# Performance work log

Hardware: AMD Instinct MI355X
Metric: run time of the kernel (lower is better)

## Reference

```python
import jax, jax.numpy as jnp
import numpy as np

DIM = 1024
DIM_HEAD = 128
HEADS = 8
DIM_INNER = DIM_HEAD * HEADS


def setup_inputs() -> dict:
    key = jax.random.key(0)
    k_x, k_qkv, k_out = jax.random.split(key, 3)
    x = jax.random.normal(k_x, (2, 2048, DIM), dtype=jnp.float32)
    gamma = jnp.ones((DIM,), dtype=jnp.float32)
    # nn.Linear weights stored as [out, in]; init ~ U(-1/sqrt(in), 1/sqrt(in))
    w_qkv = jax.random.uniform(k_qkv, (DIM_INNER * 3, DIM), dtype=jnp.float32,
                               minval=-1.0, maxval=1.0) / np.sqrt(DIM)
    w_out = jax.random.uniform(k_out, (DIM, DIM_INNER), dtype=jnp.float32,
                               minval=-1.0, maxval=1.0) / np.sqrt(DIM_INNER)
    return {"x": x, "gamma": gamma, "w_qkv": w_qkv, "w_out": w_out}


def reference(x, gamma, w_qkv, w_out):
    scale_norm = DIM ** 0.5
    scale_attn = DIM_HEAD ** -0.5
    # RMSNorm as written: F.normalize (L2) * sqrt(dim) * gamma
    l2 = jnp.sqrt(jnp.sum(x * x, axis=-1, keepdims=True))
    xn = x / jnp.maximum(l2, 1e-12) * scale_norm * gamma
    # QKV projection: [b, n, 3*h*d]
    qkv = jnp.einsum('bnc,fc->bnf', xn, w_qkv)
    b, n, _ = qkv.shape
    qkv = qkv.reshape(b, n, 3, HEADS, DIM_HEAD)
    q, k, v = (qkv[:, :, 0], qkv[:, :, 1], qkv[:, :, 2])  # [b, n, h, d]
    q = q * scale_attn
    sim = jnp.einsum('bihd,bjhd->bhij', q, k)
    causal_mask = jnp.triu(jnp.ones((n, n), dtype=bool), k=1)
    neg = -jnp.finfo(sim.dtype).max
    sim = jnp.where(causal_mask, neg, sim)
    attn = jax.nn.softmax(sim, axis=-1)
    out = jnp.einsum('bhij,bjhd->bihd', attn, v)
    out = out.reshape(b, n, DIM_INNER)  # merge heads: b n (h d)
    return jnp.einsum('bnf,cf->bnc', out, w_out)
```

## Files before the change

### kernel.cpp

```cpp
#include <hip/hip_runtime.h>

#define SEQ 2048
#define NTOK 4096
#define DIM 1024
#define FQKV 3072
#define SC_Q (0.08838834764831843f * 1.4426950408889634f)
#define SC_NORM 32.0f

typedef short short8 __attribute__((ext_vector_type(8)));
typedef float f32x4 __attribute__((ext_vector_type(4)));
typedef unsigned short u16x4 __attribute__((ext_vector_type(4)));

__device__ __forceinline__ unsigned short f2bf(float f) {
    unsigned int u = __float_as_uint(f);
    u += 0x7fffu + ((u >> 16) & 1u);
    return (unsigned short)(u >> 16);
}
__device__ __forceinline__ float bf2f(unsigned short b) {
    return __uint_as_float(((unsigned int)b) << 16);
}
__device__ __forceinline__ void gl_lds16(const void* g, void* l) {
    __builtin_amdgcn_global_load_lds((const __attribute__((address_space(1))) void*)g,
                                     (__attribute__((address_space(3))) void*)l, 16, 0, 0);
}

__global__ __launch_bounds__(256) void prep(const float* __restrict__ x,
                                            const float* __restrict__ gamma,
                                            unsigned short* __restrict__ xn,
                                            const float* __restrict__ wq,
                                            unsigned short* __restrict__ wqb,
                                            const float* __restrict__ wo,
                                            unsigned short* __restrict__ wob) {
    if (blockIdx.x < 4096) {
        int token = blockIdx.x;
        float4 v = ((const float4*)(x + (size_t)token * DIM))[threadIdx.x];
        float ss = v.x * v.x + v.y * v.y + v.z * v.z + v.w * v.w;
#pragma unroll
        for (int off = 32; off > 0; off >>= 1) ss += __shfl_down(ss, off);
        __shared__ float wsum[4];
        if ((threadIdx.x & 63) == 0) wsum[threadIdx.x >> 6] = ss;
        __syncthreads();
        float tot = wsum[0] + wsum[1] + wsum[2] + wsum[3];
        float sc = SC_NORM / fmaxf(sqrtf(tot), 1e-12f);
        float4 g = ((const float4*)gamma)[threadIdx.x];
        u16x4 o;
        o.x = f2bf(v.x * sc * g.x);
        o.y = f2bf(v.y * sc * g.y);
        o.z = f2bf(v.z * sc * g.z);
        o.w = f2bf(v.w * sc * g.w);
        ((u16x4*)(xn + (size_t)token * DIM))[threadIdx.x] = o;
    } else {
        int i = (blockIdx.x - 4096) * 256 + threadIdx.x;
        const float* w; unsigned short* o; int idx;
        if (i < 786432) { w = wq; o = wqb; idx = i; }
        else            { w = wo; o = wob; idx = i - 786432; }
        float4 v = ((const float4*)w)[idx];
        u16x4 r;
        r.x = f2bf(v.x); r.y = f2bf(v.y); r.z = f2bf(v.z); r.w = f2bf(v.w);
        ((u16x4*)o)[idx] = r;
    }
}

template<int C_MODE, int TM>
__global__ __launch_bounds__(256) void gemm_bf16(const unsigned short* __restrict__ A,
                                                 const unsigned short* __restrict__ B,
                                                 void* __restrict__ Cv,
                                                 int M, int N, int K) {
    constexpr int MF = TM / 32;
    __shared__ unsigned short As[TM * 64];
    __shared__ unsigned short Bs[128 * 64];

    int lin = blockIdx.y * gridDim.x + blockIdx.x;
    int nwg = gridDim.x * gridDim.y;
    int w = (lin & 7) * (nwg >> 3) + (lin >> 3);
    int bx = w % gridDim.x, by = w / gridDim.x;

    const int bn = bx * 128, bm = by * TM;
    const int tid = threadIdx.x, lane = tid & 63, wv = tid >> 6;
    const int wr = wv >> 1, wc = wv & 1;
    const int l15 = lane & 15, g = lane >> 4;

    f32x4 acc[MF][4] = {};

    auto stage = [&](int k0) {
#pragma unroll
        for (int ia = 0; ia < TM / 32; ++ia) {
            int ci = ia * 256 + wv * 64 + lane;
            int row = ci >> 3, cc = ci & 7;
            int co = (cc ^ (row & 7)) << 3;
            gl_lds16(A + (size_t)(bm + row) * K + k0 + co, &As[(ia * 256 + wv * 64) * 8]);
        }
#pragma unroll
        for (int ib = 0; ib < 4; ++ib) {
            int ci = ib * 256 + wv * 64 + lane;
            int row = ci >> 3, cc = ci & 7;
            int co = (cc ^ (row & 7)) << 3;
            gl_lds16(B + (size_t)(bn + row) * K + k0 + co, &Bs[(ib * 256 + wv * 64) * 8]);
        }
    };

    stage(0);
    asm volatile("s_waitcnt vmcnt(0)\ns_barrier" ::: "memory");

    for (int k0 = 0; k0 < K; k0 += 64) {
        short8 af[2][MF], bf[2][4];
#pragma unroll
        for (int ks = 0; ks < 2; ++ks) {
#pragma unroll
            for (int f = 0; f < MF; ++f) {
                int ra = wr * (TM / 2) + f * 16 + l15;
                af[ks][f] = *(const short8*)&As[ra * 64 + (((ks * 4 + g) ^ (ra & 7)) << 3)];
            }
#pragma unroll
            for (int f = 0; f < 4; ++f) {
                int rb = wc * 64 + f * 16 + l15;
                bf[ks][f] = *(const short8*)&Bs[rb * 64 + (((ks * 4 + g) ^ (rb & 7)) << 3)];
            }
        }
        asm volatile("s_waitcnt lgkmcnt(0)\ns_barrier" ::: "memory");
        if (k0 + 64 < K) stage(k0 + 64);
#pragma unroll
        for (int ks = 0; ks < 2; ++ks)
#pragma unroll
            for (int i = 0; i < MF; ++i)
#pragma unroll
                for (int j = 0; j < 4; ++j)
                    acc[i][j] = __builtin_amdgcn_mfma_f32_16x16x32_bf16(af[ks][i], bf[ks][j], acc[i][j], 0, 0, 0);
        asm volatile("s_waitcnt vmcnt(0)\ns_barrier" ::: "memory");
    }

    if (C_MODE == 0) {
        float* C = (float*)Cv;
#pragma unroll
        for (int i = 0; i < MF; ++i)
#pragma unroll
            for (int j = 0; j < 4; ++j)
#pragma unroll
                for (int v = 0; v < 4; ++v) {
                    int row = bm + wr * (TM / 2) + i * 16 + g * 4 + v;
                    int col = bn + wc * 64 + j * 16 + l15;
                    C[(size_t)row * N + col] = acc[i][j][v];
                }
    } else {
        unsigned short* C = (unsigned short*)Cv;
        float s = (bn < 1024) ? SC_Q : 1.0f;
#pragma unroll
        for (int i = 0; i < MF; ++i)
#pragma unroll
            for (int j = 0; j < 4; ++j)
#pragma unroll
                for (int v = 0; v < 4; ++v) {
                    int row = bm + wr * (TM / 2) + i * 16 + g * 4 + v;
                    int col = bn + wc * 64 + j * 16 + l15;
                    C[(size_t)row * N + col] = f2bf(acc[i][j][v] * s);
                }
    }
}

__global__ __launch_bounds__(256) void transpose_v(const unsigned short* __restrict__ qkv,
                                                   unsigned short* __restrict__ vt) {
    __shared__ unsigned short T[64][72];
    const int t0 = blockIdx.x * 64, d0 = blockIdx.y * 64, bh = blockIdx.z;
    const int b = bh >> 3, h = bh & 7;
    const int tid = threadIdx.x;
#pragma unroll
    for (int p = 0; p < 2; ++p) {
        int r = p * 32 + (tid >> 3), c = tid & 7;
        *(short8*)&T[r][c * 8] =
            *(const short8*)(qkv + (size_t)(b * SEQ + t0 + r) * FQKV + 2048 + h * 128 + d0 + c * 8);
    }
    __syncthreads();
#pragma unroll
    for (int p = 0; p < 2; ++p) {
        int d = p * 32 + (tid >> 3), c = tid & 7;
        short8 v;
#pragma unroll
        for (int j = 0; j < 8; ++j) v[j] = (short)T[c * 8 + j][d];
        *(short8*)(vt + (size_t)(bh * 128 + d0 + d) * SEQ + t0 + c * 8) = v;
    }
}

__global__ __launch_bounds__(256) void attn_mfma(const unsigned short* __restrict__ qkv,
                                                 const unsigned short* __restrict__ vt,
                                                 unsigned short* __restrict__ ao,
                                                 unsigned short* __restrict__ po,
                                                 float* __restrict__ pml) {
    __shared__ unsigned short Ks[64 * 128];
    __shared__ unsigned short Vs[128 * 64];
    __shared__ unsigned short Ps[4][16 * 64];
    const int h = blockIdx.y, b = blockIdx.z;
    const int x = blockIdx.x;
    int qblk, s, nsp;
    if (x < 30)      { qblk = 27 - x / 3;               s = x % 3;  nsp = 3; }
    else if (x < 46) { int i = x - 30; qblk = 31 - (i >> 2); s = i & 3; nsp = 4; }
    else if (x < 64) { int i = x - 46; qblk = 17 - (i >> 1); s = i & 1; nsp = 2; }
    else             { qblk = 72 - x;                   s = 0;      nsp = 1; }
    const int T = qblk + 1;
    const int jb0 = (s * T) / nsp, jb1 = ((s + 1) * T) / nsp;
    const int split = (nsp > 1);
    const int slot = ((b * 8 + h) << 6) + x;

    const int tid = threadIdx.x, lane = tid & 63, wv = tid >> 6;
    const int l15 = lane & 15, g = lane >> 4;
    const int q0 = qblk * 64;
    const int qrow = q0 + wv * 16 + l15;

    auto stageK = [&](int jb) {
#pragma unroll
        for (int inst = 0; inst < 4; ++inst) {
            int ci = inst * 256 + wv * 64 + lane;
            int rowk = ci >> 4, ck = ci & 15;
            gl_lds16(qkv + (size_t)(b * SEQ + jb * 64 + rowk) * FQKV + 1024 + h * 128
                         + ((ck ^ (rowk & 7)) << 3),
                     &Ks[(inst * 256 + wv * 64) * 8]);
        }
    };
    auto stageV = [&](int jb) {
#pragma unroll
        for (int inst = 0; inst < 4; ++inst) {
            int ci = inst * 256 + wv * 64 + lane;
            int rowv = ci >> 3, cv = ci & 7;
            gl_lds16(vt + (size_t)((b * 8 + h) * 128 + rowv) * SEQ + jb * 64
                        + ((cv ^ (rowv & 7)) << 3),
                     &Vs[(inst * 256 + wv * 64) * 8]);
        }
    };

    short8 qf[4];
    {
        const unsigned short* qb = qkv + (size_t)(b * SEQ + qrow) * FQKV + h * 128;
#pragma unroll
        for (int ks = 0; ks < 4; ++ks) qf[ks] = *(const short8*)(qb + ks * 32 + g * 8);
    }

    float m_r = -1e30f, l_r = 0.f;
    f32x4 o[8] = {};

    stageK(jb0);
    __syncthreads();

    for (int jb = jb0; jb < jb1; ++jb) {
        stageV(jb);

        f32x4 sv[4] = {};
        __builtin_amdgcn_s_setprio(1);
#pragma unroll
        for (int ks = 0; ks < 4; ++ks) {
#pragma unroll
            for (int fi = 0; fi < 4; ++fi) {
                int rk = fi * 16 + l15;
                short8 kf = *(const short8*)&Ks[rk * 128 + (((ks * 4 + g) ^ (rk & 7)) << 3)];
                sv[fi] = __builtin_amdgcn_mfma_f32_16x16x32_bf16(kf, qf[ks], sv[fi], 0, 0, 0);
            }
        }
        __builtin_amdgcn_s_setprio(0);

        if (jb == qblk) {
#pragma unroll
            for (int fi = 0; fi < 4; ++fi)
#pragma unroll
                for (int v = 0; v < 4; ++v) {
                    int kv = q0 + fi * 16 + g * 4 + v;
                    if (kv > qrow) sv[fi][v] = -1e30f;
                }
        }

        float mx = -1e30f;
#pragma unroll
        for (int fi = 0; fi < 4; ++fi)
            mx = fmaxf(mx, fmaxf(fmaxf(sv[fi][0], sv[fi][1]), fmaxf(sv[fi][2], sv[fi][3])));
        mx = fmaxf(mx, __shfl_xor(mx, 16));
        mx = fmaxf(mx, __shfl_xor(mx, 32));
        if (__any(mx - m_r > 16.0f)) {
            float Mn = fmaxf(m_r, mx);
            float alpha = exp2f(m_r - Mn);
            l_r *= alpha;
            float av[4];
#pragma unroll
            for (int v = 0; v < 4; ++v) av[v] = __shfl(alpha, g * 4 + v);
#pragma unroll
            for (int fn = 0; fn < 8; ++fn) {
                o[fn][0] *= av[0]; o[fn][1] *= av[1]; o[fn][2] *= av[2]; o[fn][3] *= av[3];
            }
            m_r = Mn;
        }

        float ps = 0.f;
#pragma unroll
        for (int fi = 0; fi < 4; ++fi) {
#pragma unroll
            for (int p2 = 0; p2 < 2; ++p2) {
                float e0 = exp2f(sv[fi][2 * p2] - m_r);
                float e1 = exp2f(sv[fi][2 * p2 + 1] - m_r);
                ps += e0 + e1;
                unsigned short b0 = f2bf(e0), b1 = f2bf(e1);
                int kv = fi * 16 + g * 4 + 2 * p2;
                int addr = l15 * 64 + (((kv >> 3) ^ (l15 & 7)) << 3) + (kv & 7);
                *(unsigned int*)&Ps[wv][addr] = (unsigned int)b0 | ((unsigned int)b1 << 16);
            }
        }
        ps += __shfl_xor(ps, 16);
        ps += __shfl_xor(ps, 32);
        l_r += ps;

        __syncthreads();
        if (jb + 1 < jb1) stageK(jb + 1);

        __builtin_amdgcn_s_setprio(1);
#pragma unroll
        for (int ks = 0; ks < 2; ++ks) {
            short8 pa = *(const short8*)&Ps[wv][l15 * 64 + (((ks * 4 + g) ^ (l15 & 7)) << 3)];
#pragma unroll
            for (int fn = 0; fn < 8; ++fn) {
                int rv = fn * 16 + l15;
                short8 vf = *(const short8*)&Vs[rv * 64 + (((ks * 4 + g) ^ (rv & 7)) << 3)];
                o[fn] = __builtin_amdgcn_mfma_f32_16x16x32_bf16(pa, vf, o[fn], 0, 0, 0);
            }
        }
        __builtin_amdgcn_s_setprio(0);

        __syncthreads();
    }

    if (split) {
        unsigned short* od = po + (size_t)slot * 8192;
#pragma unroll
        for (int fn = 0; fn < 8; ++fn)
#pragma unroll
            for (int v = 0; v < 4; ++v)
                od[(wv * 16 + g * 4 + v) * 128 + fn * 16 + l15] = f2bf(o[fn][v]);
        if (g == 0) {
            pml[(size_t)slot * 128 + wv * 16 + l15] = m_r;
            pml[(size_t)slot * 128 + 64 + wv * 16 + l15] = l_r;
        }
    } else {
        float lv[4];
#pragma unroll
        for (int v = 0; v < 4; ++v) lv[v] = 1.0f / __shfl(l_r, g * 4 + v);
#pragma unroll
        for (int fn = 0; fn < 8; ++fn)
#pragma unroll
            for (int v = 0; v < 4; ++v) {
                int row = b * SEQ + q0 + wv * 16 + g * 4 + v;
                ao[(size_t)row * DIM + h * 128 + fn * 16 + l15] = f2bf(o[fn][v] * lv[v]);
            }
    }
}

__global__ __launch_bounds__(256) void attn_combine(const unsigned short* __restrict__ po,
                                                    const float* __restrict__ pml,
                                                    unsigned short* __restrict__ ao) {
    const int qblk = 9 + blockIdx.x, h = blockIdx.y, b = blockIdx.z;
    int base, n;
    if (qblk >= 28)      { base = 30 + (31 - qblk) * 4; n = 4; }
    else if (qblk >= 18) { base = (27 - qblk) * 3;      n = 3; }
    else                 { base = 46 + (17 - qblk) * 2; n = 2; }
    const int slot0 = ((b * 8 + h) << 6) + base;
    const int row = threadIdx.x >> 2, dp = threadIdx.x & 3;

    float M = -1e30f;
#pragma unroll
    for (int s2 = 0; s2 < 4; ++s2)
        if (s2 < n) M = fmaxf(M, pml[(size_t)(slot0 + s2) * 128 + row]);
    float denom = 0.f;
#pragma unroll
    for (int s2 = 0; s2 < 4; ++s2)
        if (s2 < n) denom += exp2f(pml[(size_t)(slot0 + s2) * 128 + row] - M)
                             * pml[(size_t)(slot0 + s2) * 128 + 64 + row];
    float inv = 1.0f / denom;

    float acc[32] = {};
#pragma unroll
    for (int s2 = 0; s2 < 4; ++s2)
        if (s2 < n) {
            float wgt = exp2f(pml[(size_t)(slot0 + s2) * 128 + row] - M) * inv;
            const unsigned short* ob = po + (size_t)(slot0 + s2) * 8192 + row * 128 + dp * 32;
#pragma unroll
            for (int j = 0; j < 4; ++j) {
                short8 pv = *(const short8*)(ob + j * 8);
#pragma unroll
                for (int e = 0; e < 8; ++e)
                    acc[j * 8 + e] += wgt * bf2f((unsigned short)pv[e]);
            }
        }

    unsigned short* dst = ao + ((size_t)(b * SEQ + qblk * 64 + row)) * DIM + h * 128 + dp * 32;
#pragma unroll
    for (int j = 0; j < 4; ++j) {
        short8 r;
#pragma unroll
        for (int e = 0; e < 8; ++e) r[e] = (short)f2bf(acc[j * 8 + e]);
        *(short8*)(dst + j * 8) = r;
    }
}

extern "C" void kernel_launch(void* const* d_in, const int* in_sizes, int n_in,
                              void* d_out, int out_size, void* d_ws, size_t ws_size,
                              hipStream_t stream) {
    const float* x     = (const float*)d_in[0];
    const float* gamma = (const float*)d_in[1];
    const float* w_qkv = (const float*)d_in[2];
    const float* w_out = (const float*)d_in[3];

    char* ws = (char*)d_ws;
    unsigned short* qkvb = (unsigned short*)ws;
    unsigned short* vtb  = (unsigned short*)(ws + 25165824);
    unsigned short* xnb  = (unsigned short*)(ws + 33554432);
    unsigned short* wqb  = (unsigned short*)(ws + 41943040);
    unsigned short* wob  = (unsigned short*)(ws + 48234496);
    unsigned short* aob  = (unsigned short*)(ws + 50331648);
    float*          pml  = (float*)(ws + 41943040);
    unsigned short* po   = (unsigned short*)d_out;

    prep<<<8192, 256, 0, stream>>>(x, gamma, xnb, w_qkv, wqb, w_out, wob);
    gemm_bf16<1, 128><<<dim3(24, 32), 256, 0, stream>>>(xnb, wqb, qkvb, NTOK, FQKV, DIM);
    transpose_v<<<dim3(32, 2, 16), 256, 0, stream>>>(qkvb, vtb);
    attn_mfma<<<dim3(73, 8, 2), 256, 0, stream>>>(qkvb, vtb, aob, po, pml);
    attn_combine<<<dim3(23, 8, 2), 256, 0, stream>>>(po, pml, aob);
    gemm_bf16<0, 64><<<dim3(8, 64), 256, 0, stream>>>(aob, wob, (float*)d_out, NTOK, DIM, DIM);
}
```

Measured before the change: 118.2 us.

## Process 128 query rows per attention block to reuse staged K/V tiles

Each attention workgroup now handles two 64-row query subtiles (128 rows) instead of one, so each K and V tile staged in LDS feeds twice as many MFMAs. The split-K schedule and the combine kernel are remapped to 128-row super-blocks, with 36 blocks per head instead of 73. This halves K/V global-to-LDS traffic per query row. In exchange it doubles accumulator registers, which may lower occupancy, and yields fewer, coarser blocks, which may hurt load balance. It also does some extra causal masking work on the diagonal tiles.

```diff
diff --git a/kernel.cpp b/kernel.cpp
--- a/kernel.cpp
+++ b/kernel.cpp
@@ -187,23 +187,21 @@
                                                  float* __restrict__ pml) {
     __shared__ unsigned short Ks[64 * 128];
     __shared__ unsigned short Vs[128 * 64];
-    __shared__ unsigned short Ps[4][16 * 64];
+    __shared__ unsigned short Ps[4][2][16 * 64];
     const int h = blockIdx.y, b = blockIdx.z;
     const int x = blockIdx.x;
-    int qblk, s, nsp;
-    if (x < 30)      { qblk = 27 - x / 3;               s = x % 3;  nsp = 3; }
-    else if (x < 46) { int i = x - 30; qblk = 31 - (i >> 2); s = i & 3; nsp = 4; }
-    else if (x < 64) { int i = x - 46; qblk = 17 - (i >> 1); s = i & 1; nsp = 2; }
-    else             { qblk = 72 - x;                   s = 0;      nsp = 1; }
-    const int T = qblk + 1;
+    int qsb, s, nsp;
+    if (x < 24)      { qsb = 15 - x / 3;               s = x % 3;  nsp = 3; }
+    else if (x < 32) { int i = x - 24; qsb = 7 - (i >> 1); s = i & 1; nsp = 2; }
+    else             { qsb = 35 - x;                   s = 0;      nsp = 1; }
+    const int T = 2 * qsb + 2;
     const int jb0 = (s * T) / nsp, jb1 = ((s + 1) * T) / nsp;
     const int split = (nsp > 1);
-    const int slot = ((b * 8 + h) << 6) + x;
+    const int slot = ((b * 8 + h) << 5) + x;
 
     const int tid = threadIdx.x, lane = tid & 63, wv = tid >> 6;
     const int l15 = lane & 15, g = lane >> 4;
-    const int q0 = qblk * 64;
-    const int qrow = q0 + wv * 16 + l15;
+    const int q0 = qsb * 128;
 
     auto stageK = [&](int jb) {
 #pragma unroll
@@ -226,15 +224,16 @@
         }
     };
 
-    short8 qf[4];
-    {
-        const unsigned short* qb = qkv + (size_t)(b * SEQ + qrow) * FQKV + h * 128;
-#pragma unroll
-        for (int ks = 0; ks < 4; ++ks) qf[ks] = *(const short8*)(qb + ks * 32 + g * 8);
-    }
-
-    float m_r = -1e30f, l_r = 0.f;
-    f32x4 o[8] = {};
+    short8 qf[2][4];
+#pragma unroll
+    for (int e = 0; e < 2; ++e) {
+        const unsigned short* qb = qkv + (size_t)(b * SEQ + q0 + wv * 16 + e * 64 + l15) * FQKV + h * 128;
+#pragma unroll
+        for (int ks = 0; ks < 4; ++ks) qf[e][ks] = *(const short8*)(qb + ks * 32 + g * 8);
+    }
+
+    float m_r[2] = {-1e30f, -1e30f}, l_r[2] = {0.f, 0.f};
+    f32x4 o[2][8] = {};
 
     stageK(jb0);
     __syncthreads();
@@ -242,7 +241,7 @@
     for (int jb = jb0; jb < jb1; ++jb) {
         stageV(jb);
 
-        f32x4 sv[4] = {};
+        f32x4 sv[2][4] = {};
         __builtin_amdgcn_s_setprio(1);
 #pragma unroll
         for (int ks = 0; ks < 4; ++ks) {
@@ -250,58 +249,66 @@
             for (int fi = 0; fi < 4; ++fi) {
                 int rk = fi * 16 + l15;
                 short8 kf = *(const short8*)&Ks[rk * 128 + (((ks * 4 + g) ^ (rk & 7)) << 3)];
-                sv[fi] = __builtin_amdgcn_mfma_f32_16x16x32_bf16(kf, qf[ks], sv[fi], 0, 0, 0);
+                sv[0][fi] = __builtin_amdgcn_mfma_f32_16x16x32_bf16(kf, qf[0][ks], sv[0][fi], 0, 0, 0);
+                sv[1][fi] = __builtin_amdgcn_mfma_f32_16x16x32_bf16(kf, qf[1][ks], sv[1][fi], 0, 0, 0);
             }
         }
         __builtin_amdgcn_s_setprio(0);
 
-        if (jb == qblk) {
+        if (jb >= 2 * qsb) {
+#pragma unroll
+            for (int e = 0; e < 2; ++e) {
+                int qrow = q0 + wv * 16 + e * 64 + l15;
+#pragma unroll
+                for (int fi = 0; fi < 4; ++fi)
+#pragma unroll
+                    for (int v = 0; v < 4; ++v) {
+                        int kv = jb * 64 + fi * 16 + g * 4 + v;
+                        if (kv > qrow) sv[e][fi][v] = -1e30f;
+                    }
+            }
+        }
+
+#pragma unroll
+        for (int e = 0; e < 2; ++e) {
+            float mx = -1e30f;
 #pragma unroll
             for (int fi = 0; fi < 4; ++fi)
-#pragma unroll
-                for (int v = 0; v < 4; ++v) {
-                    int kv = q0 + fi * 16 + g * 4 + v;
-                    if (kv > qrow) sv[fi][v] = -1e30f;
+                mx = fmaxf(mx, fmaxf(fmaxf(sv[e][fi][0], sv[e][fi][1]), fmaxf(sv[e][fi][2], sv[e][fi][3])));
+            mx = fmaxf(mx, __shfl_xor(mx, 16));
+            mx = fmaxf(mx, __shfl_xor(mx, 32));
+            if (__any(mx - m_r[e] > 16.0f)) {
+                float Mn = fmaxf(m_r[e], mx);
+                float alpha = exp2f(m_r[e] - Mn);
+                l_r[e] *= alpha;
+                float av[4];
+#pragma unroll
+                for (int v = 0; v < 4; ++v) av[v] = __shfl(alpha, g * 4 + v);
+#pragma unroll
+                for (int fn = 0; fn < 8; ++fn) {
+                    o[e][fn][0] *= av[0]; o[e][fn][1] *= av[1];
+                    o[e][fn][2] *= av[2]; o[e][fn][3] *= av[3];
                 }
-        }
-
-        float mx = -1e30f;
-#pragma unroll
-        for (int fi = 0; fi < 4; ++fi)
-            mx = fmaxf(mx, fmaxf(fmaxf(sv[fi][0], sv[fi][1]), fmaxf(sv[fi][2], sv[fi][3])));
-        mx = fmaxf(mx, __shfl_xor(mx, 16));
-        mx = fmaxf(mx, __shfl_xor(mx, 32));
-        if (__any(mx - m_r > 16.0f)) {
-            float Mn = fmaxf(m_r, mx);
-            float alpha = exp2f(m_r - Mn);
-            l_r *= alpha;
-            float av[4];
-#pragma unroll
-            for (int v = 0; v < 4; ++v) av[v] = __shfl(alpha, g * 4 + v);
-#pragma unroll
-            for (int fn = 0; fn < 8; ++fn) {
-                o[fn][0] *= av[0]; o[fn][1] *= av[1]; o[fn][2] *= av[2]; o[fn][3] *= av[3];
-            }
-            m_r = Mn;
-        }
-
-        float ps = 0.f;
-#pragma unroll
-        for (int fi = 0; fi < 4; ++fi) {
-#pragma unroll
-            for (int p2 = 0; p2 < 2; ++p2) {
-                float e0 = exp2f(sv[fi][2 * p2] - m_r);
-                float e1 = exp2f(sv[fi][2 * p2 + 1] - m_r);
-                ps += e0 + e1;
-                unsigned short b0 = f2bf(e0), b1 = f2bf(e1);
-                int kv = fi * 16 + g * 4 + 2 * p2;
-                int addr = l15 * 64 + (((kv >> 3) ^ (l15 & 7)) << 3) + (kv & 7);
-                *(unsigned int*)&Ps[wv][addr] = (unsigned int)b0 | ((unsigned int)b1 << 16);
-            }
-        }
-        ps += __shfl_xor(ps, 16);
-        ps += __shfl_xor(ps, 32);
-        l_r += ps;
+                m_r[e] = Mn;
+            }
+            float ps = 0.f;
+#pragma unroll
+            for (int fi = 0; fi < 4; ++fi) {
+#pragma unroll
+                for (int p2 = 0; p2 < 2; ++p2) {
+                    float e0 = exp2f(sv[e][fi][2 * p2] - m_r[e]);
+                    float e1 = exp2f(sv[e][fi][2 * p2 + 1] - m_r[e]);
+                    ps += e0 + e1;
+                    unsigned short b0 = f2bf(e0), b1 = f2bf(e1);
+                    int kv = fi * 16 + g * 4 + 2 * p2;
+                    int addr = l15 * 64 + (((kv >> 3) ^ (l15 & 7)) << 3) + (kv & 7);
+                    *(unsigned int*)&Ps[wv][e][addr] = (unsigned int)b0 | ((unsigned int)b1 << 16);
+                }
+            }
+            ps += __shfl_xor(ps, 16);
+            ps += __shfl_xor(ps, 32);
+            l_r[e] += ps;
+        }
 
         __syncthreads();
         if (jb + 1 < jb1) stageK(jb + 1);
@@ -309,12 +316,14 @@
         __builtin_amdgcn_s_setprio(1);
 #pragma unroll
         for (int ks = 0; ks < 2; ++ks) {
-            short8 pa = *(const short8*)&Ps[wv][l15 * 64 + (((ks * 4 + g) ^ (l15 & 7)) << 3)];
+            short8 pa0 = *(const short8*)&Ps[wv][0][l15 * 64 + (((ks * 4 + g) ^ (l15 & 7)) << 3)];
+            short8 pa1 = *(const short8*)&Ps[wv][1][l15 * 64 + (((ks * 4 + g) ^ (l15 & 7)) << 3)];
 #pragma unroll
             for (int fn = 0; fn < 8; ++fn) {
                 int rv = fn * 16 + l15;
                 short8 vf = *(const short8*)&Vs[rv * 64 + (((ks * 4 + g) ^ (rv & 7)) << 3)];
-                o[fn] = __builtin_amdgcn_mfma_f32_16x16x32_bf16(pa, vf, o[fn], 0, 0, 0);
+                o[0][fn] = __builtin_amdgcn_mfma_f32_16x16x32_bf16(pa0, vf, o[0][fn], 0, 0, 0);
+                o[1][fn] = __builtin_amdgcn_mfma_f32_16x16x32_bf16(pa1, vf, o[1][fn], 0, 0, 0);
             }
         }
         __builtin_amdgcn_s_setprio(0);
@@ -323,60 +332,67 @@
     }
 
     if (split) {
-        unsigned short* od = po + (size_t)slot * 8192;
-#pragma unroll
-        for (int fn = 0; fn < 8; ++fn)
-#pragma unroll
-            for (int v = 0; v < 4; ++v)
-                od[(wv * 16 + g * 4 + v) * 128 + fn * 16 + l15] = f2bf(o[fn][v]);
+        unsigned short* od = po + (size_t)slot * 16384;
+#pragma unroll
+        for (int e = 0; e < 2; ++e)
+#pragma unroll
+            for (int fn = 0; fn < 8; ++fn)
+#pragma unroll
+                for (int v = 0; v < 4; ++v)
+                    od[(wv * 16 + e * 64 + g * 4 + v) * 128 + fn * 16 + l15] = f2bf(o[e][fn][v]);
         if (g == 0) {
-            pml[(size_t)slot * 128 + wv * 16 + l15] = m_r;
-            pml[(size_t)slot * 128 + 64 + wv * 16 + l15] = l_r;
+#pragma unroll
+            for (int e = 0; e < 2; ++e) {
+                pml[(size_t)slot * 256 + wv * 16 + e * 64 + l15] = m_r[e];
+                pml[(size_t)slot * 256 + 128 + wv * 16 + e * 64 + l15] = l_r[e];
+            }
         }
     } else {
-        float lv[4];
-#pragma unroll
-        for (int v = 0; v < 4; ++v) lv[v] = 1.0f / __shfl(l_r, g * 4 + v);
-#pragma unroll
-        for (int fn = 0; fn < 8; ++fn)
-#pragma unroll
-            for (int v = 0; v < 4; ++v) {
-                int row = b * SEQ + q0 + wv * 16 + g * 4 + v;
-                ao[(size_t)row * DIM + h * 128 + fn * 16 + l15] = f2bf(o[fn][v] * lv[v]);
-            }
+#pragma unroll
+        for (int e = 0; e < 2; ++e) {
+            float lv[4];
+#pragma unroll
+            for (int v = 0; v < 4; ++v) lv[v] = 1.0f / __shfl(l_r[e], g * 4 + v);
+#pragma unroll
+            for (int fn = 0; fn < 8; ++fn)
+#pragma unroll
+                for (int v = 0; v < 4; ++v) {
+                    int row = b * SEQ + q0 + wv * 16 + e * 64 + g * 4 + v;
+                    ao[(size_t)row * DIM + h * 128 + fn * 16 + l15] = f2bf(o[e][fn][v] * lv[v]);
+                }
+        }
     }
 }
 
 __global__ __launch_bounds__(256) void attn_combine(const unsigned short* __restrict__ po,
                                                     const float* __restrict__ pml,
                                                     unsigned short* __restrict__ ao) {
-    const int qblk = 9 + blockIdx.x, h = blockIdx.y, b = blockIdx.z;
+    const int qsb = 4 + blockIdx.x, h = blockIdx.y, b = blockIdx.z;
     int base, n;
-    if (qblk >= 28)      { base = 30 + (31 - qblk) * 4; n = 4; }
-    else if (qblk >= 18) { base = (27 - qblk) * 3;      n = 3; }
-    else                 { base = 46 + (17 - qblk) * 2; n = 2; }
-    const int slot0 = ((b * 8 + h) << 6) + base;
-    const int row = threadIdx.x >> 2, dp = threadIdx.x & 3;
+    if (qsb >= 8) { base = (15 - qsb) * 3;      n = 3; }
+    else          { base = 24 + (7 - qsb) * 2;  n = 2; }
+    const int slot0 = ((b * 8 + h) << 5) + base;
+    const int row = threadIdx.x >> 1, d0 = (threadIdx.x & 1) * 64;
 
     float M = -1e30f;
 #pragma unroll
-    for (int s2 = 0; s2 < 4; ++s2)
-        if (s2 < n) M = fmaxf(M, pml[(size_t)(slot0 + s2) * 128 + row]);
+    for (int s2 = 0; s2 < 3; ++s2)
+        if (s2 < n) M = fmaxf(M, pml[(size_t)(slot0 + s2) * 256 + row]);
     float denom = 0.f;
 #pragma unroll
-    for (int s2 = 0; s2 < 4; ++s2)
-        if (s2 < n) denom += exp2f(pml[(size_t)(slot0 + s2) * 128 + row] - M)
-                             * pml[(size_t)(slot0 + s2) * 128 + 64 + row];
+    for (int s2 = 0; s2 < 3; ++s2)
+        if (s2 < n) denom += exp2f(pml[(size_t)(slot0 + s2) * 256 + row] - M)
+                             * pml[(size_t)(slot0 + s2) * 256 + 128 + row];
     float inv = 1.0f / denom;
 
-    float acc[32] = {};
-#pragma unroll
-    for (int s2 = 0; s2 < 4; ++s2)
+    float acc[64] = {};
+#pragma unroll
+    for (int s2 = 0; s2 < 3; ++s2)
         if (s2 < n) {
-            float wgt = exp2f(pml[(size_t)(slot0 + s2) * 128 + row] - M) * inv;
-            const unsigned short* ob = po + (size_t)(slot0 + s2) * 8192 + row * 128 + dp * 32;
-#pragma unroll
-            for (int j = 0; j < 4; ++j) {
+            float wgt = exp2f(pml[(size_t)(slot0 + s2) * 256 + row] - M) * inv;
+            const unsigned short* ob = po + (size_t)(slot0 + s2) * 16384 + row * 128 + d0;
+#pragma unroll
+            for (int j = 0; j < 8; ++j) {
                 short8 pv = *(const short8*)(ob + j * 8);
 #pragma unroll
                 for (int e = 0; e < 8; ++e)
@@ -384,9 +400,9 @@
             }
         }
 
-    unsigned short* dst = ao + ((size_t)(b * SEQ + qblk * 64 + row)) * DIM + h * 128 + dp * 32;
-#pragma unroll
-    for (int j = 0; j < 4; ++j) {
+    unsigned short* dst = ao + ((size_t)(b * SEQ + qsb * 128 + row)) * DIM + h * 128 + d0;
+#pragma unroll
+    for (int j = 0; j < 8; ++j) {
         short8 r;
 #pragma unroll
         for (int e = 0; e < 8; ++e) r[e] = (short)f2bf(acc[j * 8 + e]);
@@ -415,7 +431,7 @@
     prep<<<8192, 256, 0, stream>>>(x, gamma, xnb, w_qkv, wqb, w_out, wob);
     gemm_bf16<1, 128><<<dim3(24, 32), 256, 0, stream>>>(xnb, wqb, qkvb, NTOK, FQKV, DIM);
     transpose_v<<<dim3(32, 2, 16), 256, 0, stream>>>(qkvb, vtb);
-    attn_mfma<<<dim3(73, 8, 2), 256, 0, stream>>>(qkvb, vtb, aob, po, pml);
-    attn_combine<<<dim3(23, 8, 2), 256, 0, stream>>>(po, pml, aob);
+    attn_mfma<<<dim3(36, 8, 2), 256, 0, stream>>>(qkvb, vtb, aob, po, pml);
+    attn_combine<<<dim3(12, 8, 2), 256, 0, stream>>>(po, pml, aob);
     gemm_bf16<0, 64><<<dim3(8, 64), 256, 0, stream>>>(aob, wob, (float*)d_out, NTOK, DIM, DIM);
 }
```

Result: slower. 144.4 us (+22.2%).

## Switch attention to 32x32x16 MFMA with two waves per block

Applied to the files above, without the earlier changes.

The attention kernel moves from 16x16x32 to 32x32x16 bf16 MFMA tiles, using 2 waves of 32 query rows each instead of 4 waves of 16. This reduces per-wave LDS traffic for K/V fragments and removes the cross-lane shuffles for max, sum and alpha, since each lane now owns one query row. It also packs P with v_cvt_pk_bf16_f32 and stores outputs as packed pairs. The cost is fewer threads per block staging K/V tiles, more accumulator registers per lane, and a different XOR-swizzled P layout in LDS.

```diff
diff --git a/kernel.cpp b/kernel.cpp
--- a/kernel.cpp
+++ b/kernel.cpp
@@ -9,6 +9,7 @@
 
 typedef short short8 __attribute__((ext_vector_type(8)));
 typedef float f32x4 __attribute__((ext_vector_type(4)));
+typedef float f32x16 __attribute__((ext_vector_type(16)));
 typedef unsigned short u16x4 __attribute__((ext_vector_type(4)));
 
 __device__ __forceinline__ unsigned short f2bf(float f) {
@@ -180,14 +181,14 @@
     }
 }
 
-__global__ __launch_bounds__(256) void attn_mfma(const unsigned short* __restrict__ qkv,
+__global__ __launch_bounds__(128) void attn_mfma(const unsigned short* __restrict__ qkv,
                                                  const unsigned short* __restrict__ vt,
                                                  unsigned short* __restrict__ ao,
                                                  unsigned short* __restrict__ po,
                                                  float* __restrict__ pml) {
     __shared__ unsigned short Ks[64 * 128];
     __shared__ unsigned short Vs[128 * 64];
-    __shared__ unsigned short Ps[4][16 * 64];
+    __shared__ unsigned int Ps[2][32 * 32];
     const int h = blockIdx.y, b = blockIdx.z;
     const int x = blockIdx.x;
     int qblk, s, nsp;
@@ -201,40 +202,40 @@
     const int slot = ((b * 8 + h) << 6) + x;
 
     const int tid = threadIdx.x, lane = tid & 63, wv = tid >> 6;
-    const int l15 = lane & 15, g = lane >> 4;
+    const int q = lane & 31, hi = lane >> 5;
     const int q0 = qblk * 64;
-    const int qrow = q0 + wv * 16 + l15;
+    const int qrow = q0 + wv * 32 + q;
 
     auto stageK = [&](int jb) {
 #pragma unroll
-        for (int inst = 0; inst < 4; ++inst) {
-            int ci = inst * 256 + wv * 64 + lane;
+        for (int inst = 0; inst < 8; ++inst) {
+            int ci = inst * 128 + tid;
             int rowk = ci >> 4, ck = ci & 15;
             gl_lds16(qkv + (size_t)(b * SEQ + jb * 64 + rowk) * FQKV + 1024 + h * 128
                          + ((ck ^ (rowk & 7)) << 3),
-                     &Ks[(inst * 256 + wv * 64) * 8]);
+                     &Ks[ci * 8]);
         }
     };
     auto stageV = [&](int jb) {
 #pragma unroll
-        for (int inst = 0; inst < 4; ++inst) {
-            int ci = inst * 256 + wv * 64 + lane;
+        for (int inst = 0; inst < 8; ++inst) {
+            int ci = inst * 128 + tid;
             int rowv = ci >> 3, cv = ci & 7;
             gl_lds16(vt + (size_t)((b * 8 + h) * 128 + rowv) * SEQ + jb * 64
                         + ((cv ^ (rowv & 7)) << 3),
-                     &Vs[(inst * 256 + wv * 64) * 8]);
+                     &Vs[ci * 8]);
         }
     };
 
-    short8 qf[4];
+    short8 qf[8];
     {
         const unsigned short* qb = qkv + (size_t)(b * SEQ + qrow) * FQKV + h * 128;
 #pragma unroll
-        for (int ks = 0; ks < 4; ++ks) qf[ks] = *(const short8*)(qb + ks * 32 + g * 8);
+        for (int ks = 0; ks < 8; ++ks) qf[ks] = *(const short8*)(qb + ks * 16 + hi * 8);
     }
 
     float m_r = -1e30f, l_r = 0.f;
-    f32x4 o[8] = {};
+    f32x16 o[4] = {};
 
     stageK(jb0);
     __syncthreads();
@@ -242,64 +243,60 @@
     for (int jb = jb0; jb < jb1; ++jb) {
         stageV(jb);
 
-        f32x4 sv[4] = {};
+        f32x16 sv[2] = {};
         __builtin_amdgcn_s_setprio(1);
 #pragma unroll
-        for (int ks = 0; ks < 4; ++ks) {
-#pragma unroll
-            for (int fi = 0; fi < 4; ++fi) {
-                int rk = fi * 16 + l15;
-                short8 kf = *(const short8*)&Ks[rk * 128 + (((ks * 4 + g) ^ (rk & 7)) << 3)];
-                sv[fi] = __builtin_amdgcn_mfma_f32_16x16x32_bf16(kf, qf[ks], sv[fi], 0, 0, 0);
+        for (int ks = 0; ks < 8; ++ks) {
+#pragma unroll
+            for (int fi = 0; fi < 2; ++fi) {
+                int rk = fi * 32 + q;
+                short8 kf = *(const short8*)&Ks[rk * 128 + (((ks * 2 + hi) ^ (rk & 7)) << 3)];
+                sv[fi] = __builtin_amdgcn_mfma_f32_32x32x16_bf16(kf, qf[ks], sv[fi], 0, 0, 0);
             }
         }
         __builtin_amdgcn_s_setprio(0);
 
         if (jb == qblk) {
 #pragma unroll
-            for (int fi = 0; fi < 4; ++fi)
-#pragma unroll
-                for (int v = 0; v < 4; ++v) {
-                    int kv = q0 + fi * 16 + g * 4 + v;
-                    if (kv > qrow) sv[fi][v] = -1e30f;
+            for (int fi = 0; fi < 2; ++fi)
+#pragma unroll
+                for (int r = 0; r < 16; ++r) {
+                    int kv = jb * 64 + fi * 32 + (r & 3) + 8 * (r >> 2) + 4 * hi;
+                    if (kv > qrow) sv[fi][r] = -1e30f;
                 }
         }
 
         float mx = -1e30f;
 #pragma unroll
-        for (int fi = 0; fi < 4; ++fi)
-            mx = fmaxf(mx, fmaxf(fmaxf(sv[fi][0], sv[fi][1]), fmaxf(sv[fi][2], sv[fi][3])));
-        mx = fmaxf(mx, __shfl_xor(mx, 16));
+        for (int fi = 0; fi < 2; ++fi)
+#pragma unroll
+            for (int r = 0; r < 16; ++r) mx = fmaxf(mx, sv[fi][r]);
         mx = fmaxf(mx, __shfl_xor(mx, 32));
         if (__any(mx - m_r > 16.0f)) {
             float Mn = fmaxf(m_r, mx);
             float alpha = exp2f(m_r - Mn);
             l_r *= alpha;
-            float av[4];
-#pragma unroll
-            for (int v = 0; v < 4; ++v) av[v] = __shfl(alpha, g * 4 + v);
-#pragma unroll
-            for (int fn = 0; fn < 8; ++fn) {
-                o[fn][0] *= av[0]; o[fn][1] *= av[1]; o[fn][2] *= av[2]; o[fn][3] *= av[3];
-            }
+#pragma unroll
+            for (int fd = 0; fd < 4; ++fd)
+#pragma unroll
+                for (int r = 0; r < 16; ++r) o[fd][r] *= alpha;
             m_r = Mn;
         }
 
         float ps = 0.f;
 #pragma unroll
-        for (int fi = 0; fi < 4; ++fi) {
-#pragma unroll
-            for (int p2 = 0; p2 < 2; ++p2) {
-                float e0 = exp2f(sv[fi][2 * p2] - m_r);
-                float e1 = exp2f(sv[fi][2 * p2 + 1] - m_r);
+        for (int fi = 0; fi < 2; ++fi) {
+#pragma unroll
+            for (int rp = 0; rp < 8; ++rp) {
+                float e0 = exp2f(sv[fi][2 * rp] - m_r);
+                float e1 = exp2f(sv[fi][2 * rp + 1] - m_r);
                 ps += e0 + e1;
-                unsigned short b0 = f2bf(e0), b1 = f2bf(e1);
-                int kv = fi * 16 + g * 4 + 2 * p2;
-                int addr = l15 * 64 + (((kv >> 3) ^ (l15 & 7)) << 3) + (kv & 7);
-                *(unsigned int*)&Ps[wv][addr] = (unsigned int)b0 | ((unsigned int)b1 << 16);
-            }
-        }
-        ps += __shfl_xor(ps, 16);
+                unsigned int pk;
+                asm("v_cvt_pk_bf16_f32 %0, %1, %2" : "=v"(pk) : "v"(e0), "v"(e1));
+                int kvp = (rp & 1) + ((rp >> 1) << 2) + 2 * hi + fi * 16;
+                Ps[wv][q * 32 + (kvp ^ ((q & 7) << 2))] = pk;
+            }
+        }
         ps += __shfl_xor(ps, 32);
         l_r += ps;
 
@@ -308,13 +305,14 @@
 
         __builtin_amdgcn_s_setprio(1);
 #pragma unroll
-        for (int ks = 0; ks < 2; ++ks) {
-            short8 pa = *(const short8*)&Ps[wv][l15 * 64 + (((ks * 4 + g) ^ (l15 & 7)) << 3)];
-#pragma unroll
-            for (int fn = 0; fn < 8; ++fn) {
-                int rv = fn * 16 + l15;
-                short8 vf = *(const short8*)&Vs[rv * 64 + (((ks * 4 + g) ^ (rv & 7)) << 3)];
-                o[fn] = __builtin_amdgcn_mfma_f32_16x16x32_bf16(pa, vf, o[fn], 0, 0, 0);
+        for (int c = 0; c < 4; ++c) {
+            short8 pb = *(const short8*)((const unsigned short*)
+                            &Ps[wv][q * 32 + (((c * 8 + hi * 4)) ^ ((q & 7) << 2))]);
+#pragma unroll
+            for (int fd = 0; fd < 4; ++fd) {
+                int rv = fd * 32 + q;
+                short8 vf = *(const short8*)&Vs[rv * 64 + (((c * 2 + hi) ^ (rv & 7)) << 3)];
+                o[fd] = __builtin_amdgcn_mfma_f32_32x32x16_bf16(vf, pb, o[fd], 0, 0, 0);
             }
         }
         __builtin_amdgcn_s_setprio(0);
@@ -325,24 +323,31 @@
     if (split) {
         unsigned short* od = po + (size_t)slot * 8192;
 #pragma unroll
-        for (int fn = 0; fn < 8; ++fn)
-#pragma unroll
-            for (int v = 0; v < 4; ++v)
-                od[(wv * 16 + g * 4 + v) * 128 + fn * 16 + l15] = f2bf(o[fn][v]);
-        if (g == 0) {
-            pml[(size_t)slot * 128 + wv * 16 + l15] = m_r;
-            pml[(size_t)slot * 128 + 64 + wv * 16 + l15] = l_r;
+        for (int fd = 0; fd < 4; ++fd)
+#pragma unroll
+            for (int rp = 0; rp < 8; ++rp) {
+                float e0 = o[fd][2 * rp], e1 = o[fd][2 * rp + 1];
+                unsigned int pk;
+                asm("v_cvt_pk_bf16_f32 %0, %1, %2" : "=v"(pk) : "v"(e0), "v"(e1));
+                int d = fd * 32 + ((2 * rp) & 3) + 8 * (rp >> 1) + 4 * hi;
+                *(unsigned int*)(od + (wv * 32 + q) * 128 + d) = pk;
+            }
+        if (hi == 0) {
+            pml[(size_t)slot * 128 + wv * 32 + q] = m_r;
+            pml[(size_t)slot * 128 + 64 + wv * 32 + q] = l_r;
         }
     } else {
-        float lv[4];
-#pragma unroll
-        for (int v = 0; v < 4; ++v) lv[v] = 1.0f / __shfl(l_r, g * 4 + v);
-#pragma unroll
-        for (int fn = 0; fn < 8; ++fn)
-#pragma unroll
-            for (int v = 0; v < 4; ++v) {
-                int row = b * SEQ + q0 + wv * 16 + g * 4 + v;
-                ao[(size_t)row * DIM + h * 128 + fn * 16 + l15] = f2bf(o[fn][v] * lv[v]);
+        float inv = 1.0f / l_r;
+        unsigned short* dst = ao + (size_t)(b * SEQ + qrow) * DIM + h * 128;
+#pragma unroll
+        for (int fd = 0; fd < 4; ++fd)
+#pragma unroll
+            for (int rp = 0; rp < 8; ++rp) {
+                float e0 = o[fd][2 * rp] * inv, e1 = o[fd][2 * rp + 1] * inv;
+                unsigned int pk;
+                asm("v_cvt_pk_bf16_f32 %0, %1, %2" : "=v"(pk) : "v"(e0), "v"(e1));
+                int d = fd * 32 + ((2 * rp) & 3) + 8 * (rp >> 1) + 4 * hi;
+                *(unsigned int*)(dst + d) = pk;
             }
     }
 }
@@ -415,7 +420,7 @@
     prep<<<8192, 256, 0, stream>>>(x, gamma, xnb, w_qkv, wqb, w_out, wob);
     gemm_bf16<1, 128><<<dim3(24, 32), 256, 0, stream>>>(xnb, wqb, qkvb, NTOK, FQKV, DIM);
     transpose_v<<<dim3(32, 2, 16), 256, 0, stream>>>(qkvb, vtb);
-    attn_mfma<<<dim3(73, 8, 2), 256, 0, stream>>>(qkvb, vtb, aob, po, pml);
+    attn_mfma<<<dim3(73, 8, 2), 128, 0, stream>>>(qkvb, vtb, aob, po, pml);
     attn_combine<<<dim3(23, 8, 2), 256, 0, stream>>>(po, pml, aob);
     gemm_bf16<0, 64><<<dim3(8, 64), 256, 0, stream>>>(aob, wob, (float*)d_out, NTOK, DIM, DIM);
 }
```

After: 133.0 us. 1.12x slower.
